# Optimization experiments

Measured on AMD Instinct MI355X. Metric: run time of the kernel, lower is better.

Reference implementation:

```python
import jax, jax.numpy as jnp
import numpy as np

B, T, SZ, H = 16, 512, 512, 8
HD = SZ // H
D0, STD, GAMMA = 6.3, 1.4, 2.0
MAX_RPE = 16

def _dwconv(x, w):
    # depthwise conv1d, kernel 5, pad 2, groups=C, no bias; x: [B,T,C], w: [C,1,5]
    y = jax.lax.conv_general_dilated(x.transpose(0, 2, 1), w, (1,), [(2, 2)],
        dimension_numbers=('NCH', 'OIH', 'NCH'), feature_group_count=x.shape[-1])
    return y.transpose(0, 2, 1)

def _forward(mask, key, value, query, Wq, bq, Wk, bk, Wv, bv, Wcq, Wck, Wcv, Wgq, bgq, Wgk, bgk, Wgv, bgv, WmD, bmD, rpe_table, Wo, bo):
    q = query @ Wq.T + bq
    k = key @ Wk.T + bk
    v = value @ Wv.T + bv
    xn = key  # x_norm := key in the original forward
    # gated depthwise-conv context injection (qkv_context=[1,1,1], fuse='gate')
    qc = _dwconv(xn, Wcq)
    g = jax.nn.sigmoid(jnp.concatenate([q, qc], -1) @ Wgq.T + bgq)
    q = (1 - g) * q + g * qc
    kc = _dwconv(xn, Wck)
    g = jax.nn.sigmoid(jnp.concatenate([k, kc], -1) @ Wgk.T + bgk)
    k = (1 - g) * k + g * kc
    vc = _dwconv(xn, Wcv)
    g = jax.nn.sigmoid(jnp.concatenate([v, vc], -1) @ Wgv.T + bgv)
    v = (1 - g) * v + g * vc
    # learned Gaussian width: mod_D='head_share', mod_src='Q'
    off = (q @ WmD.T + bmD)[..., 0]                       # [B,T]
    m_D = D0 + 2.0 * STD * jnp.tanh(off / GAMMA)          # [B,T]
    qh = q.reshape(B, T, H, HD).transpose(0, 2, 1, 3) / jnp.sqrt(jnp.float32(HD))
    kh = k.reshape(B, T, H, HD).transpose(0, 2, 1, 3)
    vh = v.reshape(B, T, H, HD).transpose(0, 2, 1, 3)
    scores = jnp.einsum('bhqd,bhkd->bhqk', qh, kh)        # [B,H,T,T]
    idx = jnp.arange(T)
    d_int = idx[:, None] - idx[None, :]                   # i - j
    rd = jnp.clip(-d_int, -MAX_RPE, MAX_RPE) + MAX_RPE    # rpe indices [T,T]
    rpe = rpe_table[rd]                                   # [T,T,2*HD]
    rpe_k, rpe_v = rpe[..., :HD], rpe[..., HD:]
    scores = scores + jnp.einsum('bhqd,qkd->bhqk', qh, rpe_k)
    dist = d_int.astype(jnp.float32)
    scores = scores - dist ** 2 / (m_D[:, None, :, None] ** 2 / 2.0)
    scores = jnp.where(mask[:, None, :, :], -jnp.inf, scores)
    attn = jax.nn.softmax(scores, axis=-1)                # dropout is identity at eval
    ctx = jnp.einsum('bhqk,bhkd->bhqd', attn, vh) + jnp.einsum('bhqk,qkd->bhqd', attn, rpe_v)
    out = ctx.transpose(0, 2, 1, 3).reshape(B, T, SZ) @ Wo.T + bo
    return out

def setup_inputs():
    rng = jax.random.key(0)
    ks = jax.random.split(rng, 20)
    s = 0.02
    lin = lambda k, o, i: jax.random.normal(k, (o, i), jnp.float32) * s
    lengths = jax.random.randint(ks[3], (B,), T // 2, T + 1)
    mask = (jnp.arange(T)[None, :] >= lengths[:, None])[:, None, :]  # [B,1,T], True = pad
    return {
        'key': jax.random.normal(ks[0], (B, T, SZ), jnp.float32),
        'value': jax.random.normal(ks[1], (B, T, SZ), jnp.float32),
        'query': jax.random.normal(ks[2], (B, T, SZ), jnp.float32),
        'mask': mask,
        'Wq': lin(ks[4], SZ, SZ), 'bq': jnp.zeros((SZ,), jnp.float32),
        'Wk': lin(ks[5], SZ, SZ), 'bk': jnp.zeros((SZ,), jnp.float32),
        'Wv': lin(ks[6], SZ, SZ), 'bv': jnp.zeros((SZ,), jnp.float32),
        'Wcq': jax.random.normal(ks[7], (SZ, 1, 5), jnp.float32) * s,
        'Wck': jax.random.normal(ks[8], (SZ, 1, 5), jnp.float32) * s,
        'Wcv': jax.random.normal(ks[9], (SZ, 1, 5), jnp.float32) * s,
        'Wgq': lin(ks[10], 1, 2 * SZ), 'bgq': jnp.zeros((1,), jnp.float32),
        'Wgk': lin(ks[11], 1, 2 * SZ), 'bgk': jnp.zeros((1,), jnp.float32),
        'Wgv': lin(ks[12], 1, 2 * SZ), 'bgv': jnp.zeros((1,), jnp.float32),
        'WmD': lin(ks[13], 1, SZ), 'bmD': jnp.zeros((1,), jnp.float32),
        'rpe_table': jax.random.normal(ks[14], (2 * MAX_RPE + 1, 2 * HD), jnp.float32) * s,
        'Wo': lin(ks[15], SZ, SZ), 'bo': jnp.zeros((SZ,), jnp.float32),
    }

def reference(key, value, query, mask, Wq, bq, Wk, bk, Wv, bv, Wcq, Wck, Wcv, Wgq, bgq, Wgk, bgk, Wgv, bgv, WmD, bmD, rpe_table, Wo, bo):
    return _forward(mask, key, value, query, Wq, bq, Wk, bk, Wv, bv, Wcq, Wck, Wcv, Wgq, bgq, Wgk, bgk, Wgv, bgv, WmD, bmD, rpe_table, Wo, bo)
```

## Files before the change

### kernel.cpp

```cpp
#include <hip/hip_runtime.h>
#include <math.h>

#define NB 16
#define NT 512
#define NSZ 512
#define NH 8
#define NHD 64
#define MAXR 16

#define C_D0 6.3f
#define C_STD 1.4f
#define C_GAMMA 2.0f

#define NEGINF (-1e30f)
#define LOG2E 1.4426950408889634f
#define C1F   0.18033688011112042f

typedef unsigned short u16;
typedef __attribute__((ext_vector_type(8))) short bf16x8;
typedef __attribute__((ext_vector_type(4))) float f32x4;
typedef __attribute__((ext_vector_type(8))) unsigned short u16x8;

__device__ __forceinline__ u16 f2b(float f) {
    union { float f; unsigned int u; } c; c.f = f;
    unsigned int u = c.u + 0x7FFFu + ((c.u >> 16) & 1u);
    return (u16)(u >> 16);
}
__device__ __forceinline__ float b2f(u16 h) {
    union { unsigned int u; float f; } c; c.u = ((unsigned int)h) << 16;
    return c.f;
}

#if __has_builtin(__builtin_amdgcn_exp2f)
__device__ __forceinline__ float exp2_fast(float x) { return __builtin_amdgcn_exp2f(x); }
#else
__device__ __forceinline__ float exp2_fast(float x) { return exp2f(x); }
#endif

#define GL2LDS(gp, lp) __builtin_amdgcn_global_load_lds( \
    (const __attribute__((address_space(1))) void*)(gp), \
    (__attribute__((address_space(3))) void*)(lp), 16, 0, 0)

#define SWU(r, c) ((((r) * 8) + ((c) ^ ((r) & 7))) * 8)
#define SWU16(r, c) ((((r) * 16) + ((c) ^ ((r) & 7))) * 8)

__global__ __launch_bounds__(256) void cvt4_bf16(
    const float* __restrict__ s0, const float* __restrict__ s1,
    const float* __restrict__ s2, const float* __restrict__ s3,
    u16* __restrict__ d0, u16* __restrict__ d1,
    u16* __restrict__ d2, u16* __restrict__ d3, int n)
{
    const float* s; u16* d;
    switch (blockIdx.y) {
        case 0: s = s0; d = d0; break;
        case 1: s = s1; d = d1; break;
        case 2: s = s2; d = d2; break;
        default: s = s3; d = d3; break;
    }
    int i = (blockIdx.x * 256 + threadIdx.x) * 8;
    if (i >= n) return;
    float4 a = *(const float4*)&s[i];
    float4 b = *(const float4*)&s[i + 4];
    u16x8 v;
    v[0]=f2b(a.x); v[1]=f2b(a.y); v[2]=f2b(a.z); v[3]=f2b(a.w);
    v[4]=f2b(b.x); v[5]=f2b(b.y); v[6]=f2b(b.z); v[7]=f2b(b.w);
    *(u16x8*)&d[i] = v;
}

__global__ __launch_bounds__(256) void wprep(
    const float* __restrict__ Wcq, const float* __restrict__ Wck,
    const float* __restrict__ Wcv, float* __restrict__ WcT)
{
    const int z = blockIdx.y;
    const float* src = z == 0 ? Wcq : (z == 1 ? Wck : Wcv);
    int idx = blockIdx.x * 256 + threadIdx.x;
    if (idx >= 2560) return;
    int c = idx / 5, j = idx % 5;
    WcT[(size_t)z * 2560 + j * 512 + c] = src[idx];
}

__global__ __launch_bounds__(256) void gemm_qkv(
    const float* __restrict__ A0, const float* __restrict__ A1, const float* __restrict__ A2,
    const u16* __restrict__ Wc,
    const float* __restrict__ bq, const float* __restrict__ bk, const float* __restrict__ bv,
    u16* __restrict__ pkv)
{
    __shared__ u16 Al[2][64 * 32];
    __shared__ u16 Bl[2][128 * 32];
    const int z = blockIdx.z;
    const float* A = z == 0 ? A0 : (z == 1 ? A1 : A2);
    const u16* W = Wc + (size_t)z * NSZ * NSZ;
    const float* bias = z == 0 ? bq : (z == 1 ? bk : bv);
    const int tid = threadIdx.x;
    const int m0 = blockIdx.x * 64;
    const int n0 = blockIdx.y * 128;
    const int w = tid >> 6, lane = tid & 63;
    const int wm = (w >> 1) * 32, wn = (w & 1) * 64;
    const int fr = lane & 15, fk = lane >> 4;

    const int arow = tid >> 2, acb = tid & 3;
    const int wrow0 = tid >> 2, wcb = tid & 3;

    f32x4 acc[2][4] = {};

    {
        const float* ga = &A[(size_t)(m0 + arow) * NSZ + acb * 8];
        float4 a0 = *(const float4*)ga, a1 = *(const float4*)(ga + 4);
        #pragma unroll
        for (int p = 0; p < 2; ++p) {
            int s = tid + p * 256;
            int row = s >> 2, cb = s & 3;
            GL2LDS(&W[(size_t)(n0 + row) * NSZ + cb * 8], &Bl[0][s * 8]);
        }
        u16x8 v;
        v[0]=f2b(a0.x); v[1]=f2b(a0.y); v[2]=f2b(a0.z); v[3]=f2b(a0.w);
        v[4]=f2b(a1.x); v[5]=f2b(a1.y); v[6]=f2b(a1.z); v[7]=f2b(a1.w);
        *(u16x8*)&Al[0][tid * 8] = v;
    }
    __syncthreads();

    for (int t = 0; t < 16; ++t) {
        const int cur = t & 1, nxt = cur ^ 1;
        float4 a0n, a1n;
        const bool pre = (t < 15);
        if (pre) {
            const int k0 = (t + 1) * 32;
            const float* ga = &A[(size_t)(m0 + arow) * NSZ + k0 + acb * 8];
            a0n = *(const float4*)ga;
            a1n = *(const float4*)(ga + 4);
            #pragma unroll
            for (int p = 0; p < 2; ++p) {
                int s = tid + p * 256;
                int row = s >> 2, cb = s & 3;
                GL2LDS(&W[(size_t)(n0 + row) * NSZ + k0 + cb * 8], &Bl[nxt][s * 8]);
            }
        }
        bf16x8 af[2], bfr[4];
        #pragma unroll
        for (int mf = 0; mf < 2; ++mf)
            af[mf] = *(const bf16x8*)&Al[cur][(wm + mf * 16 + fr) * 32 + fk * 8];
        #pragma unroll
        for (int nf = 0; nf < 4; ++nf)
            bfr[nf] = *(const bf16x8*)&Bl[cur][(wn + nf * 16 + fr) * 32 + fk * 8];
        #pragma unroll
        for (int mf = 0; mf < 2; ++mf)
            #pragma unroll
            for (int nf = 0; nf < 4; ++nf)
                acc[mf][nf] = __builtin_amdgcn_mfma_f32_16x16x32_bf16(
                    af[mf], bfr[nf], acc[mf][nf], 0, 0, 0);
        if (pre) {
            u16x8 v;
            v[0]=f2b(a0n.x); v[1]=f2b(a0n.y); v[2]=f2b(a0n.z); v[3]=f2b(a0n.w);
            v[4]=f2b(a1n.x); v[5]=f2b(a1n.y); v[6]=f2b(a1n.z); v[7]=f2b(a1n.w);
            *(u16x8*)&Al[nxt][tid * 8] = v;
        }
        __syncthreads();
    }
    #pragma unroll
    for (int mf = 0; mf < 2; ++mf) {
        #pragma unroll
        for (int nf = 0; nf < 4; ++nf) {
            int col = n0 + wn + nf * 16 + fr;
            float bvv = bias[col];
            #pragma unroll
            for (int r = 0; r < 4; ++r) {
                int rowg = m0 + wm + mf * 16 + fk * 4 + r;
                pkv[(size_t)rowg * 1536 + z * 512 + col] = f2b(acc[mf][nf][r] + bvv);
            }
        }
    }
}

__global__ __launch_bounds__(256) void gemm_out(
    const u16* __restrict__ A, const u16* __restrict__ W,
    const float* __restrict__ bias, float* __restrict__ Cout, int M, int N, int K)
{
    __shared__ u16 Al[2][64 * 32];
    __shared__ u16 Bl[2][128 * 32];
    const int tid = threadIdx.x;
    const int m0 = blockIdx.x * 64;
    const int n0 = blockIdx.y * 128;
    const int w = tid >> 6, lane = tid & 63;
    const int wm = (w >> 1) * 32, wn = (w & 1) * 64;
    const int fr = lane & 15, fk = lane >> 4;

    f32x4 acc[2][4] = {};

    {
        int row = tid >> 2, cb = tid & 3;
        GL2LDS(&A[(size_t)(m0 + row) * K + cb * 8], &Al[0][tid * 8]);
        #pragma unroll
        for (int p = 0; p < 2; ++p) {
            int s = tid + p * 256;
            int r2 = s >> 2, c2 = s & 3;
            GL2LDS(&W[(size_t)(n0 + r2) * K + c2 * 8], &Bl[0][s * 8]);
        }
    }
    __syncthreads();

    const int nsteps = K / 32;
    for (int t = 0; t < nsteps; ++t) {
        const int cur = t & 1, nxt = cur ^ 1;
        if (t + 1 < nsteps) {
            const int k0 = (t + 1) * 32;
            int row = tid >> 2, cb = tid & 3;
            GL2LDS(&A[(size_t)(m0 + row) * K + k0 + cb * 8], &Al[nxt][tid * 8]);
            #pragma unroll
            for (int p = 0; p < 2; ++p) {
                int s = tid + p * 256;
                int r2 = s >> 2, c2 = s & 3;
                GL2LDS(&W[(size_t)(n0 + r2) * K + k0 + c2 * 8], &Bl[nxt][s * 8]);
            }
        }
        bf16x8 af[2], bfr[4];
        #pragma unroll
        for (int mf = 0; mf < 2; ++mf)
            af[mf] = *(const bf16x8*)&Al[cur][(wm + mf * 16 + fr) * 32 + fk * 8];
        #pragma unroll
        for (int nf = 0; nf < 4; ++nf)
            bfr[nf] = *(const bf16x8*)&Bl[cur][(wn + nf * 16 + fr) * 32 + fk * 8];
        #pragma unroll
        for (int mf = 0; mf < 2; ++mf)
            #pragma unroll
            for (int nf = 0; nf < 4; ++nf)
                acc[mf][nf] = __builtin_amdgcn_mfma_f32_16x16x32_bf16(
                    af[mf], bfr[nf], acc[mf][nf], 0, 0, 0);
        __syncthreads();
    }
    #pragma unroll
    for (int mf = 0; mf < 2; ++mf) {
        #pragma unroll
        for (int nf = 0; nf < 4; ++nf) {
            int col = n0 + wn + nf * 16 + fr;
            float bv = bias[col];
            #pragma unroll
            for (int r = 0; r < 4; ++r) {
                int rowg = m0 + wm + mf * 16 + fk * 4 + r;
                Cout[(size_t)rowg * N + col] = acc[mf][nf][r] + bv;
            }
        }
    }
}

__global__ void conv_gate_all(
    const float* __restrict__ xn, u16* __restrict__ pkv,
    const float* __restrict__ WcT,
    const float* __restrict__ Wgq, const float* __restrict__ bgq,
    const float* __restrict__ Wgk, const float* __restrict__ bgk,
    const float* __restrict__ Wgv, const float* __restrict__ bgv,
    const float* __restrict__ WmD, const float* __restrict__ bmD,
    float* __restrict__ mD)
{
    const int w = threadIdx.x >> 6, lane = threadIdx.x & 63;
    const int bt = blockIdx.x * 4 + w;
    const int b = bt >> 9, tpos = bt & (NT - 1);
    const int c0 = lane * 8;

    float x[5][8];
    #pragma unroll
    for (int j = 0; j < 5; ++j) {
        int tt = tpos + j - 2;
        if (tt >= 0 && tt < NT) {
            const float4* xp = (const float4*)&xn[((size_t)(b*NT + tt))*NSZ + c0];
            float4 u0 = xp[0], u1 = xp[1];
            x[j][0]=u0.x; x[j][1]=u0.y; x[j][2]=u0.z; x[j][3]=u0.w;
            x[j][4]=u1.x; x[j][5]=u1.y; x[j][6]=u1.z; x[j][7]=u1.w;
        } else {
            #pragma unroll
            for (int i = 0; i < 8; ++i) x[j][i] = 0.f;
        }
    }
    float aq[8] = {}, ak[8] = {}, av[8] = {};
    #pragma unroll
    for (int j = 0; j < 5; ++j) {
        const float* wq = &WcT[j * 512 + c0];
        const float* wk = &WcT[2560 + j * 512 + c0];
        const float* wv = &WcT[5120 + j * 512 + c0];
        float4 q0 = *(const float4*)wq, q1 = *(const float4*)(wq + 4);
        float4 k0 = *(const float4*)wk, k1 = *(const float4*)(wk + 4);
        float4 v0 = *(const float4*)wv, v1 = *(const float4*)(wv + 4);
        float wq8[8] = {q0.x,q0.y,q0.z,q0.w,q1.x,q1.y,q1.z,q1.w};
        float wk8[8] = {k0.x,k0.y,k0.z,k0.w,k1.x,k1.y,k1.z,k1.w};
        float wv8[8] = {v0.x,v0.y,v0.z,v0.w,v1.x,v1.y,v1.z,v1.w};
        #pragma unroll
        for (int i = 0; i < 8; ++i) {
            aq[i] += x[j][i] * wq8[i];
            ak[i] += x[j][i] * wk8[i];
            av[i] += x[j][i] * wv8[i];
        }
    }
    const size_t rb = (size_t)bt * 1536;
    u16x8 q8 = *(const u16x8*)&pkv[rb + c0];
    u16x8 k8 = *(const u16x8*)&pkv[rb + 512 + c0];
    u16x8 v8 = *(const u16x8*)&pkv[rb + 1024 + c0];

    float gql[8], gqh[8], gkl[8], gkh[8], gvl[8], gvh[8];
    {
        float4 a0 = *(const float4*)&Wgq[c0],      a1 = *(const float4*)&Wgq[c0 + 4];
        float4 a2 = *(const float4*)&Wgq[512 + c0], a3 = *(const float4*)&Wgq[512 + c0 + 4];
        gql[0]=a0.x;gql[1]=a0.y;gql[2]=a0.z;gql[3]=a0.w;gql[4]=a1.x;gql[5]=a1.y;gql[6]=a1.z;gql[7]=a1.w;
        gqh[0]=a2.x;gqh[1]=a2.y;gqh[2]=a2.z;gqh[3]=a2.w;gqh[4]=a3.x;gqh[5]=a3.y;gqh[6]=a3.z;gqh[7]=a3.w;
        float4 b0 = *(const float4*)&Wgk[c0],      b1 = *(const float4*)&Wgk[c0 + 4];
        float4 b2 = *(const float4*)&Wgk[512 + c0], b3 = *(const float4*)&Wgk[512 + c0 + 4];
        gkl[0]=b0.x;gkl[1]=b0.y;gkl[2]=b0.z;gkl[3]=b0.w;gkl[4]=b1.x;gkl[5]=b1.y;gkl[6]=b1.z;gkl[7]=b1.w;
        gkh[0]=b2.x;gkh[1]=b2.y;gkh[2]=b2.z;gkh[3]=b2.w;gkh[4]=b3.x;gkh[5]=b3.y;gkh[6]=b3.z;gkh[7]=b3.w;
        float4 c0v = *(const float4*)&Wgv[c0],      c1v = *(const float4*)&Wgv[c0 + 4];
        float4 c2v = *(const float4*)&Wgv[512 + c0], c3v = *(const float4*)&Wgv[512 + c0 + 4];
        gvl[0]=c0v.x;gvl[1]=c0v.y;gvl[2]=c0v.z;gvl[3]=c0v.w;gvl[4]=c1v.x;gvl[5]=c1v.y;gvl[6]=c1v.z;gvl[7]=c1v.w;
        gvh[0]=c2v.x;gvh[1]=c2v.y;gvh[2]=c2v.z;gvh[3]=c2v.w;gvh[4]=c3v.x;gvh[5]=c3v.y;gvh[6]=c3v.z;gvh[7]=c3v.w;
    }
    float sq = 0.f, sk = 0.f, sv = 0.f;
    #pragma unroll
    for (int i = 0; i < 8; ++i) {
        sq += b2f(q8[i]) * gql[i] + aq[i] * gqh[i];
        sk += b2f(k8[i]) * gkl[i] + ak[i] * gkh[i];
        sv += b2f(v8[i]) * gvl[i] + av[i] * gvh[i];
    }
    #pragma unroll
    for (int o = 1; o < 64; o <<= 1) {
        sq += __shfl_xor(sq, o, 64);
        sk += __shfl_xor(sk, o, 64);
        sv += __shfl_xor(sv, o, 64);
    }
    float gq = 1.f / (1.f + expf(-(sq + bgq[0])));
    float gk = 1.f / (1.f + expf(-(sk + bgk[0])));
    float gv = 1.f / (1.f + expf(-(sv + bgv[0])));

    float wm8[8];
    {
        float4 m0 = *(const float4*)&WmD[c0], m1 = *(const float4*)&WmD[c0 + 4];
        wm8[0]=m0.x;wm8[1]=m0.y;wm8[2]=m0.z;wm8[3]=m0.w;wm8[4]=m1.x;wm8[5]=m1.y;wm8[6]=m1.z;wm8[7]=m1.w;
    }
    u16x8 oq8, ok8, ov8;
    float smd = 0.f;
    #pragma unroll
    for (int i = 0; i < 8; ++i) {
        float oq = (1.f - gq) * b2f(q8[i]) + gq * aq[i];
        oq8[i] = f2b(oq);
        ok8[i] = f2b((1.f - gk) * b2f(k8[i]) + gk * ak[i]);
        ov8[i] = f2b((1.f - gv) * b2f(v8[i]) + gv * av[i]);
        smd += oq * wm8[i];
    }
    *(u16x8*)&pkv[rb + c0]        = oq8;
    *(u16x8*)&pkv[rb + 512 + c0]  = ok8;
    *(u16x8*)&pkv[rb + 1024 + c0] = ov8;
    #pragma unroll
    for (int o = 1; o < 64; o <<= 1) smd += __shfl_xor(smd, o, 64);
    if (lane == 0)
        mD[bt] = C_D0 + 2.f * C_STD * tanhf((smd + bmD[0]) / C_GAMMA);
}

__global__ __launch_bounds__(256) void vtrans(
    const u16* __restrict__ pkv, u16* __restrict__ vpT)
{
    __shared__ u16 lt[64][72];
    const int t0 = blockIdx.x * 64;
    const int h = blockIdx.y, b = blockIdx.z;
    const int tid = threadIdx.x;
    #pragma unroll
    for (int p = 0; p < 2; ++p) {
        int s = tid + p * 256;
        int t = s >> 3, c8 = s & 7;
        u16x8 v = *(const u16x8*)&pkv[((size_t)(b*NT + t0 + t))*1536 + 1024 + h*NHD + c8*8];
        *(u16x8*)&lt[t][c8 * 8] = v;
    }
    __syncthreads();
    #pragma unroll
    for (int p = 0; p < 2; ++p) {
        int s = tid + p * 256;
        int d = s >> 3, c8 = s & 7;
        u16x8 o;
        #pragma unroll
        for (int j = 0; j < 8; ++j) o[j] = lt[c8 * 8 + j][d];
        *(u16x8*)&vpT[((size_t)((b*NH + h)*NHD + d))*NT + t0 + c8*8] = o;
    }
}

__global__ __launch_bounds__(256) void attn_mfma(
    const u16* __restrict__ pkv, const u16* __restrict__ vpT,
    const float* __restrict__ mD, const int* __restrict__ mask,
    const float* __restrict__ rpe, u16* __restrict__ cxh)
{
    __shared__ __align__(16) char smem[70400];
    u16*  Ql    = (u16*)(smem);
    u16*  Kl    = (u16*)(smem + 8192);
    u16*  Vl    = (u16*)(smem + 24576);
    u16*  Pl    = (u16*)(smem + 40960);
    u16*  rpk   = (u16*)(smem + 40960);
    u16*  wA16  = (u16*)(smem + 57344);
    u16*  qdrl  = (u16*)(smem + 65536);
    float* inv2s= (float*)(smem + 70144);

    const int tid  = threadIdx.x;
    const int lane = tid & 63;
    const int w    = tid >> 6;
    const int wq0  = w * 16;
    const int fr   = lane & 15;
    const int fq   = lane >> 4;
    const int b    = blockIdx.x >> 3;
    const int h    = blockIdx.x & 7;
    const int q0   = blockIdx.y * 64;

    const size_t qbase  = ((size_t)(b*NT + q0)) * 1536 + h * NHD;
    const size_t kbaseg = ((size_t)b * NT) * 1536 + 512 + h * NHD;
    const size_t vbaseg = ((size_t)((b*NH + h) * NHD)) * NT;

    int Lm = 512;
    #pragma unroll
    for (int j = 0; j < 8; ++j) {
        if (mask[b * NT + lane + 64 * j]) Lm = min(Lm, lane + 64 * j);
    }
    #pragma unroll
    for (int o = 1; o < 64; o <<= 1) Lm = min(Lm, __shfl_xor(Lm, o, 64));
    const int L = Lm;
    const int w0 = max(0, min(q0 - 32, L - 128));

    #pragma unroll
    for (int p = 0; p < 2; ++p) {
        int s = tid + p * 256;
        int r = s >> 3, c = s & 7;
        u16x8 v = *(const u16x8*)(pkv + qbase + (size_t)r * 1536 + c * 8);
        *(u16x8*)(Ql + SWU(r, c)) = v;
    }
    #pragma unroll
    for (int p = 0; p < 4; ++p) {
        int s = tid + p * 256;
        int r = s >> 3, c = s & 7;
        u16x8 v = *(const u16x8*)(pkv + kbaseg + (size_t)(w0 + r) * 1536 + c * 8);
        *(u16x8*)(Kl + SWU(r, c)) = v;
    }
    #pragma unroll
    for (int p = 0; p < 4; ++p) {
        int s = tid + p * 256;
        int d = s >> 4, cc = s & 15;
        u16x8 v = *(const u16x8*)(vpT + vbaseg + (size_t)d * NT + w0 + cc * 8);
        *(u16x8*)(Vl + SWU16(d, cc)) = v;
    }
    for (int idx = tid; idx < 264; idx += 256) {
        int r = idx >> 3, c = idx & 7;
        float4 f0 = *(const float4*)&rpe[r * 128 + c * 8];
        float4 f1 = *(const float4*)&rpe[r * 128 + c * 8 + 4];
        u16x8 vv;
        vv[0]=f2b(f0.x); vv[1]=f2b(f0.y); vv[2]=f2b(f0.z); vv[3]=f2b(f0.w);
        vv[4]=f2b(f1.x); vv[5]=f2b(f1.y); vv[6]=f2b(f1.z); vv[7]=f2b(f1.w);
        *(u16x8*)(rpk + SWU(r, c)) = vv;
    }
    if (tid < 120) {
        u16x8 vv = {0,0,0,0,0,0,0,0};
        *(u16x8*)(rpk + (((33 + (tid >> 3)) * 8) + (tid & 7)) * 8) = vv;
    }
    {
        u16x8 z = {0,0,0,0,0,0,0,0};
        #pragma unroll
        for (int p = 0; p < 2; ++p) *(u16x8*)(wA16 + (tid + p * 256) * 8) = z;
    }
    if (tid < 64) {
        float md = mD[b * NT + q0 + tid];
        inv2s[tid] = 2.f * LOG2E / (md * md);
    }
    __syncthreads();

    bf16x8 aq0 = *(const bf16x8*)(Ql + SWU(wq0 + fr, fq));
    bf16x8 aq1 = *(const bf16x8*)(Ql + SWU(wq0 + fr, 4 + fq));

    {
        f32x4 qd[3] = {};
        #pragma unroll
        for (int nf = 0; nf < 3; ++nf) {
            bf16x8 b0 = *(const bf16x8*)(rpk + SWU(nf * 16 + fr, fq));
            bf16x8 b1 = *(const bf16x8*)(rpk + SWU(nf * 16 + fr, 4 + fq));
            qd[nf] = __builtin_amdgcn_mfma_f32_16x16x32_bf16(aq0, b0, qd[nf], 0, 0, 0);
            qd[nf] = __builtin_amdgcn_mfma_f32_16x16x32_bf16(aq1, b1, qd[nf], 0, 0, 0);
        }
        #pragma unroll
        for (int nf = 0; nf < 3; ++nf) {
            int rd = nf * 16 + fr;
            if (rd < 33) {
                #pragma unroll
                for (int r = 0; r < 4; ++r)
                    qdrl[(wq0 + fq * 4 + r) * 36 + rd] = f2b(qd[nf][r]);
            }
        }
    }
    __syncthreads();

    f32x4 s_[8] = {};
    #pragma unroll
    for (int nf = 0; nf < 8; ++nf) {
        bf16x8 b0 = *(const bf16x8*)(Kl + SWU(nf * 16 + fr, fq));
        bf16x8 b1 = *(const bf16x8*)(Kl + SWU(nf * 16 + fr, 4 + fq));
        s_[nf] = __builtin_amdgcn_mfma_f32_16x16x32_bf16(aq0, b0, s_[nf], 0, 0, 0);
        s_[nf] = __builtin_amdgcn_mfma_f32_16x16x32_bf16(aq1, b1, s_[nf], 0, 0, 0);
    }

    float li[4];
    #pragma unroll
    for (int r = 0; r < 4; ++r) {
        const int lq = wq0 + fq * 4 + r;
        const int qg = q0 + lq;
        const float iv = inv2s[lq];
        float sc[8];
        float mx = NEGINF;
        #pragma unroll
        for (int nf = 0; nf < 8; ++nf) {
            const int kg = w0 + nf * 16 + fr;
            float v;
            if (kg >= L) v = NEGINF;
            else {
                int rd = min(max(kg - qg, -MAXR), MAXR) + MAXR;
                float qr = b2f(qdrl[lq * 36 + rd]);
                float fd = (float)(qg - kg);
                v = (s_[nf][r] + qr) * C1F - fd * fd * iv;
            }
            sc[nf] = v;
            mx = fmaxf(mx, v);
        }
        mx = fmaxf(mx, __shfl_xor(mx, 1, 64));
        mx = fmaxf(mx, __shfl_xor(mx, 2, 64));
        mx = fmaxf(mx, __shfl_xor(mx, 4, 64));
        mx = fmaxf(mx, __shfl_xor(mx, 8, 64));
        float rsum = 0.f, ls = 0.f, rs = 0.f;
        #pragma unroll
        for (int nf = 0; nf < 8; ++nf) {
            const int kg = w0 + nf * 16 + fr;
            float pv = exp2_fast(sc[nf] - mx);
            s_[nf][r] = pv;
            rsum += pv;
            int d = kg - qg;
            if (d <= -MAXR) ls += pv;
            else if (d >= MAXR) rs += pv;
            else {
                int bkt = d + MAXR;
                wA16[(lq * 8 + ((bkt >> 3) ^ (lq & 7))) * 8 + (bkt & 7)] = f2b(pv);
            }
        }
        rsum += __shfl_xor(rsum, 1, 64); rsum += __shfl_xor(rsum, 2, 64);
        rsum += __shfl_xor(rsum, 4, 64); rsum += __shfl_xor(rsum, 8, 64);
        ls += __shfl_xor(ls, 1, 64); ls += __shfl_xor(ls, 2, 64);
        ls += __shfl_xor(ls, 4, 64); ls += __shfl_xor(ls, 8, 64);
        rs += __shfl_xor(rs, 1, 64); rs += __shfl_xor(rs, 2, 64);
        rs += __shfl_xor(rs, 4, 64); rs += __shfl_xor(rs, 8, 64);
        li[r] = rsum;
        if (fr == 0) {
            wA16[(lq * 8 + (0 ^ (lq & 7))) * 8 + 0] = f2b(ls);
            wA16[(lq * 8 + (4 ^ (lq & 7))) * 8 + 0] = f2b(rs);
        }
    }

    #pragma unroll
    for (int r = 0; r < 4; ++r) {
        int lq = wq0 + fq * 4 + r;
        #pragma unroll
        for (int nf = 0; nf < 8; ++nf) {
            int k = nf * 16 + fr;
            int cc = k >> 3;
            Pl[(lq * 16 + (cc ^ (lq & 7))) * 8 + (k & 7)] = f2b(s_[nf][r]);
        }
    }

    f32x4 O[4] = {};
    #pragma unroll
    for (int ks = 0; ks < 4; ++ks) {
        bf16x8 ap = *(const bf16x8*)(Pl + ((wq0 + fr) * 16 + ((ks * 4 + fq) ^ (fr & 7))) * 8);
        #pragma unroll
        for (int nf = 0; nf < 4; ++nf) {
            bf16x8 vf = *(const bf16x8*)(Vl + ((nf * 16 + fr) * 16 + ((ks * 4 + fq) ^ (fr & 7))) * 8);
            O[nf] = __builtin_amdgcn_mfma_f32_16x16x32_bf16(ap, vf, O[nf], 0, 0, 0);
        }
    }
    __syncthreads();

    #pragma unroll
    for (int p = 0; p < 2; ++p) {
        int s = tid + p * 256;
        int d = s >> 3, cs = s & 7;
        u16x8 vv;
        #pragma unroll
        for (int j = 0; j < 8; ++j) {
            int rd = cs * 8 + j;
            vv[j] = (rd < 33) ? f2b(rpe[rd * 128 + 64 + d]) : (u16)0;
        }
        *(u16x8*)(Vl + SWU(d, cs)) = vv;
    }
    __syncthreads();

    {
        bf16x8 aw0 = *(const bf16x8*)(wA16 + SWU(wq0 + fr, fq));
        bf16x8 aw1 = *(const bf16x8*)(wA16 + SWU(wq0 + fr, 4 + fq));
        #pragma unroll
        for (int nf = 0; nf < 4; ++nf) {
            bf16x8 b0 = *(const bf16x8*)(Vl + SWU(nf * 16 + fr, fq));
            bf16x8 b1 = *(const bf16x8*)(Vl + SWU(nf * 16 + fr, 4 + fq));
            O[nf] = __builtin_amdgcn_mfma_f32_16x16x32_bf16(aw0, b0, O[nf], 0, 0, 0);
            O[nf] = __builtin_amdgcn_mfma_f32_16x16x32_bf16(aw1, b1, O[nf], 0, 0, 0);
        }
    }
    float invl[4];
    #pragma unroll
    for (int r = 0; r < 4; ++r) invl[r] = 1.f / li[r];
    #pragma unroll
    for (int r = 0; r < 4; ++r) {
        int lq = wq0 + fq * 4 + r;
        #pragma unroll
        for (int nf = 0; nf < 4; ++nf)
            Pl[lq * 64 + nf * 16 + fr] = f2b(O[nf][r] * invl[r]);
    }
    __syncthreads();
    #pragma unroll
    for (int j = 0; j < 2; ++j) {
        int s = w * 128 + j * 64 + lane;
        int rr = s >> 3, c8 = s & 7;
        u16x8 vv = *(const u16x8*)(Pl + rr * 64 + c8 * 8);
        *(u16x8*)&cxh[((size_t)(b*NT + q0 + rr)) * 512 + h * NHD + c8 * 8] = vv;
    }
}

extern "C" void kernel_launch(void* const* d_in, const int* in_sizes, int n_in,
                              void* d_out, int out_size, void* d_ws, size_t ws_size,
                              hipStream_t stream) {
    const float* key   = (const float*)d_in[0];
    const float* value = (const float*)d_in[1];
    const float* query = (const float*)d_in[2];
    const int*   mask  = (const int*)d_in[3];
    const float* Wq  = (const float*)d_in[4];
    const float* bq  = (const float*)d_in[5];
    const float* Wk  = (const float*)d_in[6];
    const float* bk  = (const float*)d_in[7];
    const float* Wv  = (const float*)d_in[8];
    const float* bv  = (const float*)d_in[9];
    const float* Wcq = (const float*)d_in[10];
    const float* Wck = (const float*)d_in[11];
    const float* Wcv = (const float*)d_in[12];
    const float* Wgq = (const float*)d_in[13];
    const float* bgq = (const float*)d_in[14];
    const float* Wgk = (const float*)d_in[15];
    const float* bgk = (const float*)d_in[16];
    const float* Wgv = (const float*)d_in[17];
    const float* bgv = (const float*)d_in[18];
    const float* WmD = (const float*)d_in[19];
    const float* bmD = (const float*)d_in[20];
    const float* rpe = (const float*)d_in[21];
    const float* Wo  = (const float*)d_in[22];
    const float* bo  = (const float*)d_in[23];
    float* out = (float*)d_out;

    const size_t NTOK = (size_t)NB * NT;
    const size_t NE   = NTOK * NSZ;
    const size_t NW   = (size_t)NSZ * NSZ;

    u16* ws16 = (u16*)d_ws;
    u16* pkv  = ws16;
    u16* wcat = pkv + NTOK * 1536;
    u16* woh  = wcat + 3 * NW;
    u16* vpT  = woh + NW;
    u16* cxh  = vpT + NE;
    float* mDb = (float*)(cxh + NE);
    float* WcT = mDb + NTOK;

    cvt4_bf16<<<dim3((unsigned)(NW/8/256), 4), 256, 0, stream>>>(
        Wq, Wk, Wv, Wo, wcat, wcat + NW, wcat + 2*NW, woh, (int)NW);
    wprep<<<dim3(10, 3), 256, 0, stream>>>(Wcq, Wck, Wcv, WcT);

    gemm_qkv<<<dim3(128, 4, 3), 256, 0, stream>>>(
        query, key, value, wcat, bq, bk, bv, pkv);

    conv_gate_all<<<(int)(NTOK / 4), 256, 0, stream>>>(
        key, pkv, WcT, Wgq, bgq, Wgk, bgk, Wgv, bgv, WmD, bmD, mDb);

    vtrans<<<dim3(8, 8, 16), 256, 0, stream>>>(pkv, vpT);

    attn_mfma<<<dim3(128, 8), 256, 0, stream>>>(pkv, vpT, mDb, mask, rpe, cxh);

    gemm_out<<<dim3(128, 4), 256, 0, stream>>>(cxh, woh, bo, out, (int)NTOK, NSZ, NSZ);
}
```

Before: 114.8 us.

## Fuse V transpose into conv-gate kernel and widen QKV GEMM N-tile

The gated V output is now transposed through shared memory inside conv_gate_all and written straight to the head-major vpT layout. This removes the separate vtrans kernel launch and its extra read/write of V. The QKV GEMM N-tile is also doubled from 128 to 256 columns per block, halving the grid and doubling accumulators and LDS for B. The fused transpose writes only 8-byte chunks per row, so its stores are less coalesced, and the larger GEMM tile may lower occupancy.

```diff
diff --git a/kernel.cpp b/kernel.cpp
--- a/kernel.cpp
+++ b/kernel.cpp
@@ -20,6 +20,7 @@
 typedef __attribute__((ext_vector_type(8))) short bf16x8;
 typedef __attribute__((ext_vector_type(4))) float f32x4;
 typedef __attribute__((ext_vector_type(8))) unsigned short u16x8;
+typedef __attribute__((ext_vector_type(4))) unsigned short u16x4;
 
 __device__ __forceinline__ u16 f2b(float f) {
     union { float f; unsigned int u; } c; c.f = f;
@@ -86,28 +87,27 @@
     u16* __restrict__ pkv)
 {
     __shared__ u16 Al[2][64 * 32];
-    __shared__ u16 Bl[2][128 * 32];
+    __shared__ u16 Bl[2][256 * 32];
     const int z = blockIdx.z;
     const float* A = z == 0 ? A0 : (z == 1 ? A1 : A2);
     const u16* W = Wc + (size_t)z * NSZ * NSZ;
     const float* bias = z == 0 ? bq : (z == 1 ? bk : bv);
     const int tid = threadIdx.x;
     const int m0 = blockIdx.x * 64;
-    const int n0 = blockIdx.y * 128;
+    const int n0 = blockIdx.y * 256;
     const int w = tid >> 6, lane = tid & 63;
-    const int wm = (w >> 1) * 32, wn = (w & 1) * 64;
+    const int wm = (w >> 1) * 32, wn = (w & 1) * 128;
     const int fr = lane & 15, fk = lane >> 4;
 
     const int arow = tid >> 2, acb = tid & 3;
-    const int wrow0 = tid >> 2, wcb = tid & 3;
-
-    f32x4 acc[2][4] = {};
+
+    f32x4 acc[2][8] = {};
 
     {
         const float* ga = &A[(size_t)(m0 + arow) * NSZ + acb * 8];
         float4 a0 = *(const float4*)ga, a1 = *(const float4*)(ga + 4);
         #pragma unroll
-        for (int p = 0; p < 2; ++p) {
+        for (int p = 0; p < 4; ++p) {
             int s = tid + p * 256;
             int row = s >> 2, cb = s & 3;
             GL2LDS(&W[(size_t)(n0 + row) * NSZ + cb * 8], &Bl[0][s * 8]);
@@ -129,23 +129,23 @@
             a0n = *(const float4*)ga;
             a1n = *(const float4*)(ga + 4);
             #pragma unroll
-            for (int p = 0; p < 2; ++p) {
+            for (int p = 0; p < 4; ++p) {
                 int s = tid + p * 256;
                 int row = s >> 2, cb = s & 3;
                 GL2LDS(&W[(size_t)(n0 + row) * NSZ + k0 + cb * 8], &Bl[nxt][s * 8]);
             }
         }
-        bf16x8 af[2], bfr[4];
+        bf16x8 af[2], bfr[8];
         #pragma unroll
         for (int mf = 0; mf < 2; ++mf)
             af[mf] = *(const bf16x8*)&Al[cur][(wm + mf * 16 + fr) * 32 + fk * 8];
         #pragma unroll
-        for (int nf = 0; nf < 4; ++nf)
+        for (int nf = 0; nf < 8; ++nf)
             bfr[nf] = *(const bf16x8*)&Bl[cur][(wn + nf * 16 + fr) * 32 + fk * 8];
         #pragma unroll
         for (int mf = 0; mf < 2; ++mf)
             #pragma unroll
-            for (int nf = 0; nf < 4; ++nf)
+            for (int nf = 0; nf < 8; ++nf)
                 acc[mf][nf] = __builtin_amdgcn_mfma_f32_16x16x32_bf16(
                     af[mf], bfr[nf], acc[mf][nf], 0, 0, 0);
         if (pre) {
@@ -159,7 +159,7 @@
     #pragma unroll
     for (int mf = 0; mf < 2; ++mf) {
         #pragma unroll
-        for (int nf = 0; nf < 4; ++nf) {
+        for (int nf = 0; nf < 8; ++nf) {
             int col = n0 + wn + nf * 16 + fr;
             float bvv = bias[col];
             #pragma unroll
@@ -244,6 +244,7 @@
 
 __global__ void conv_gate_all(
     const float* __restrict__ xn, u16* __restrict__ pkv,
+    u16* __restrict__ vpT,
     const float* __restrict__ WcT,
     const float* __restrict__ Wgq, const float* __restrict__ bgq,
     const float* __restrict__ Wgk, const float* __restrict__ bgk,
@@ -251,6 +252,7 @@
     const float* __restrict__ WmD, const float* __restrict__ bmD,
     float* __restrict__ mD)
 {
+    __shared__ u16 lt[4][512];
     const int w = threadIdx.x >> 6, lane = threadIdx.x & 63;
     const int bt = blockIdx.x * 4 + w;
     const int b = bt >> 9, tpos = bt & (NT - 1);
@@ -341,38 +343,23 @@
         ov8[i] = f2b((1.f - gv) * b2f(v8[i]) + gv * av[i]);
         smd += oq * wm8[i];
     }
-    *(u16x8*)&pkv[rb + c0]        = oq8;
-    *(u16x8*)&pkv[rb + 512 + c0]  = ok8;
-    *(u16x8*)&pkv[rb + 1024 + c0] = ov8;
+    *(u16x8*)&pkv[rb + c0]       = oq8;
+    *(u16x8*)&pkv[rb + 512 + c0] = ok8;
+    *(u16x8*)&lt[w][c0] = ov8;
     #pragma unroll
     for (int o = 1; o < 64; o <<= 1) smd += __shfl_xor(smd, o, 64);
     if (lane == 0)
         mD[bt] = C_D0 + 2.f * C_STD * tanhf((smd + bmD[0]) / C_GAMMA);
-}
-
-__global__ __launch_bounds__(256) void vtrans(
-    const u16* __restrict__ pkv, u16* __restrict__ vpT)
-{
-    __shared__ u16 lt[64][72];
-    const int t0 = blockIdx.x * 64;
-    const int h = blockIdx.y, b = blockIdx.z;
-    const int tid = threadIdx.x;
-    #pragma unroll
-    for (int p = 0; p < 2; ++p) {
-        int s = tid + p * 256;
-        int t = s >> 3, c8 = s & 7;
-        u16x8 v = *(const u16x8*)&pkv[((size_t)(b*NT + t0 + t))*1536 + 1024 + h*NHD + c8*8];
-        *(u16x8*)&lt[t][c8 * 8] = v;
-    }
-    __syncthreads();
-    #pragma unroll
-    for (int p = 0; p < 2; ++p) {
-        int s = tid + p * 256;
-        int d = s >> 3, c8 = s & 7;
-        u16x8 o;
-        #pragma unroll
-        for (int j = 0; j < 8; ++j) o[j] = lt[c8 * 8 + j][d];
-        *(u16x8*)&vpT[((size_t)((b*NH + h)*NHD + d))*NT + t0 + c8*8] = o;
+
+    __syncthreads();
+    const int t0g = (blockIdx.x * 4) & (NT - 1);
+    const int b0g = (blockIdx.x * 4) >> 9;
+    #pragma unroll
+    for (int p2 = 0; p2 < 2; ++p2) {
+        int c = threadIdx.x + p2 * 256;
+        u16x4 o4;
+        o4[0] = lt[0][c]; o4[1] = lt[1][c]; o4[2] = lt[2][c]; o4[3] = lt[3][c];
+        *(u16x4*)&vpT[((size_t)(b0g * 512 + c)) * NT + t0g] = o4;
     }
 }
 
@@ -661,13 +648,11 @@
         Wq, Wk, Wv, Wo, wcat, wcat + NW, wcat + 2*NW, woh, (int)NW);
     wprep<<<dim3(10, 3), 256, 0, stream>>>(Wcq, Wck, Wcv, WcT);
 
-    gemm_qkv<<<dim3(128, 4, 3), 256, 0, stream>>>(
+    gemm_qkv<<<dim3(128, 2, 3), 256, 0, stream>>>(
         query, key, value, wcat, bq, bk, bv, pkv);
 
     conv_gate_all<<<(int)(NTOK / 4), 256, 0, stream>>>(
-        key, pkv, WcT, Wgq, bgq, Wgk, bgk, Wgv, bgv, WmD, bmD, mDb);
-
-    vtrans<<<dim3(8, 8, 16), 256, 0, stream>>>(pkv, vpT);
+        key, pkv, vpT, WcT, Wgq, bgq, Wgk, bgk, Wgv, bgv, WmD, bmD, mDb);
 
     attn_mfma<<<dim3(128, 8), 256, 0, stream>>>(pkv, vpT, mDb, mask, rpe, cxh);
 
```

After: 108.6 us. 1.06x faster.
